# Performance work log

Hardware: AMD Instinct MI355X
Metric: run time of the kernel (lower is better)

## Reference

```python
import jax, jax.numpy as jnp
import numpy as np

THRESH = 8000.0  # saturating partial-sum accumulator threshold (thresh=8000 in source)
GROUP = 128      # channel chunk size used by split_tensor_* helpers
EPS = 1e-5

def binarize(x):
    # sign() forward with straight-through estimator (standard BinarizeConv2d behavior)
    return x + jax.lax.stop_gradient(jnp.sign(x) - x)

def psum_conv3x3(x, w):
    """3x3 'same' conv computed as 9 shifted-window partial sums per 128-channel
    group, with the running accumulator saturated to [-THRESH, THRESH] after each
    partial sum (emulating a low-bit hardware accumulator).
    x: [B, C, H, W]; w: [O, C, 3, 3] -> out [B, O, H, W]."""
    B, C, H, W = x.shape
    O = w.shape[0]
    xp = jnp.pad(x, ((0, 0), (0, 0), (1, 1), (1, 1)))
    acc = jnp.zeros((B, O, H, W), dtype=x.dtype)
    n_groups = C // GROUP
    for g in range(n_groups):
        xg = xp[:, g * GROUP:(g + 1) * GROUP]
        wg = w[:, g * GROUP:(g + 1) * GROUP]
        # split_tensor ordering: x1..x9 vary row (dim2) fastest, then col (dim3)
        for col in range(3):
            for row in range(3):
                part = jnp.einsum('bchw,oc->bohw',
                                  xg[:, :, row:row + H, col:col + W],
                                  wg[:, :, row, col])
                acc = jnp.clip(acc + part, -THRESH, THRESH)
    return acc

def batchnorm(x, gamma, beta, mean, var):
    inv = gamma / jnp.sqrt(var + EPS)
    return x * inv[None, :, None, None] + (beta - mean * inv)[None, :, None, None]

def setup_inputs() -> dict:
    key = jax.random.key(0)
    ks = jax.random.split(key, 12)
    B, C, H, W = 64, 128, 56, 56
    return {
        'x': jax.random.normal(ks[0], (B, C, H, W), jnp.float32),
        'w1': jax.random.normal(ks[1], (C, C, 3, 3), jnp.float32),
        'w2': jax.random.normal(ks[2], (C, C, 3, 3), jnp.float32),
        'gamma1': jax.random.uniform(ks[3], (C,), jnp.float32, 0.5, 1.5),
        'beta1': jax.random.normal(ks[4], (C,), jnp.float32) * 0.1,
        'mean1': jax.random.normal(ks[5], (C,), jnp.float32),
        'var1': jax.random.uniform(ks[6], (C,), jnp.float32, 0.5, 1.5),
        'gamma2': jax.random.uniform(ks[7], (C,), jnp.float32, 0.5, 1.5),
        'beta2': jax.random.normal(ks[8], (C,), jnp.float32) * 0.1,
        'mean2': jax.random.normal(ks[9], (C,), jnp.float32),
        'var2': jax.random.uniform(ks[10], (C,), jnp.float32, 0.5, 1.5),
    }

def reference(x, w1, w2, gamma1, beta1, mean1, var1, gamma2, beta2, mean2, var2):
    residual = x
    out = psum_conv3x3(binarize(x), binarize(w1))
    out = batchnorm(out, gamma1, beta1, mean1, var1)
    out = jnp.clip(out, -1.0, 1.0)  # hardtanh
    out = psum_conv3x3(binarize(out), binarize(w2))
    out = batchnorm(out, gamma2, beta2, mean2, var2)
    out = out + residual
    out = jnp.clip(out, -1.0, 1.0)
    return out
```

## Files before the change

kernel.cpp:

```cpp
#include <hip/hip_runtime.h>
#include <cstdint>
#include <cstddef>


typedef int      v4i __attribute__((ext_vector_type(4)));
typedef float    v4f __attribute__((ext_vector_type(4)));
typedef unsigned int v2u __attribute__((ext_vector_type(2)));

constexpr int B = 64, C = 128, H = 56, W = 56;
constexpr int HP = H + 2, WP = W + 2;
constexpr int PIX = H * W;
constexpr int M = B * H * W;
constexpr int NTILES = M / 256;
constexpr int TPX = NTILES / 8;

constexpr size_t XS_BYTES = (size_t)B * HP * WP * C;
constexpr size_t XS1_OFF = 0;
constexpr size_t XS2_OFF = XS_BYTES;
constexpr size_t WF_BYTES = 18 * 8192;
constexpr size_t WF1_OFF = 2 * XS_BYTES;
constexpr size_t WF2_OFF = WF1_OFF + WF_BYTES;
constexpr size_t BNP_OFF = WF2_OFF + WF_BYTES;

__global__ __launch_bounds__(256) void zero_halo(int8_t* __restrict__ xs1,
                                                 int8_t* __restrict__ xs2) {
    int b = blockIdx.x >> 2;
    int q = blockIdx.x & 3;
    int t = q * 256 + threadIdx.x;
    size_t ib = (size_t)b * HP * WP * C;
#pragma unroll
    for (int a = 0; a < 2; ++a) {
        uint32_t* p = (uint32_t*)((a ? xs2 : xs1) + ib);
        const int ROWD = WP * C / 4;
        for (int i = t; i < ROWD; i += 1024) {
            p[i] = 0;
            p[(HP - 1) * ROWD + i] = 0;
        }
        for (int i = t; i < 56 * 2 * 32; i += 1024) {
            int r = i >> 6;
            int side = (i >> 5) & 1;
            int j = i & 31;
            p[((r + 1) * WP + side * (WP - 1)) * (C / 4) + j] = 0;
        }
    }
}

__global__ __launch_bounds__(256) void prep_x(const float* __restrict__ x,
                                              int8_t* __restrict__ xs) {
    __shared__ uint32_t tl[256 * 33];
    int t = threadIdx.x;
    int m = blockIdx.x * 256 + t;
    int b_ = m / PIX, hw = m % PIX;
    const float* xp = x + (size_t)b_ * C * PIX + hw;
#pragma unroll
    for (int c4 = 0; c4 < 32; ++c4) {
        uint32_t v = 0;
#pragma unroll
        for (int j = 0; j < 4; ++j) {
            float f = __builtin_nontemporal_load(xp + (size_t)(c4 * 4 + j) * PIX);
            v |= ((uint32_t)(uint8_t)(int8_t)((f > 0.f) - (f < 0.f))) << (8 * j);
        }
        tl[t * 33 + c4] = v;
    }
    __syncthreads();
    int pl = t >> 3, co = t & 7;
#pragma unroll
    for (int pass = 0; pass < 8; ++pass) {
        int p = pass * 32 + pl;
        int mg = blockIdx.x * 256 + p;
        int b2 = mg / PIX, hw2 = mg % PIX, h2 = hw2 / W, w2 = hw2 % W;
        size_t ob = ((size_t)(b2 * HP + h2 + 1) * WP + (w2 + 1)) * C + co * 16;
        v4i val;
#pragma unroll
        for (int k = 0; k < 4; ++k) val[k] = (int)tl[p * 33 + co * 4 + k];
        *(v4i*)(xs + ob) = val;
    }
}

__global__ __launch_bounds__(256) void prep_w(
    const float* __restrict__ w1, const float* __restrict__ w2,
    const float* __restrict__ g1, const float* __restrict__ be1,
    const float* __restrict__ mu1, const float* __restrict__ va1,
    const float* __restrict__ g2, const float* __restrict__ be2,
    const float* __restrict__ mu2, const float* __restrict__ va2,
    int8_t* __restrict__ wf1, int8_t* __restrict__ wf2,
    float* __restrict__ bnp) {
    int t = blockIdx.x * 256 + threadIdx.x;
    if (t < 256) {
        int o = t & 127;
        if (t < 128) {
            float inv = g1[o] / sqrtf(va1[o] + 1e-5f);
            bnp[o]       = inv;
            bnp[128 + o] = __fsub_rn(be1[o], __fmul_rn(mu1[o], inv));
        } else {
            float inv = g2[o] / sqrtf(va2[o] + 1e-5f);
            bnp[256 + o] = inv;
            bnp[384 + o] = __fsub_rn(be2[o], __fmul_rn(mu2[o], inv));
        }
    }
    if (t >= 2 * 18 * 8 * 64) return;
    int lane = t & 63;
    int nsub = (t >> 6) & 7;
    int kh   = (t >> 9) & 1;
    int tap  = (t >> 10) % 9;
    int which = (t >> 10) / 9;
    const float* w = which ? w2 : w1;
    int8_t* wf = which ? wf2 : wf1;
    int o = (lane & 15) * 8 + nsub;
    int cbase = kh * 64 + (lane >> 4) * 16;
    int r = tap / 3, s = tap % 3;
    int slot = r * 6 + kh * 3 + s;
    int8_t frag[16];
#pragma unroll
    for (int j = 0; j < 16; ++j) {
        float f = w[((size_t)(o * C + cbase + j) * 3 + r) * 3 + s];
        frag[j] = (int8_t)((f > 0.f) - (f < 0.f));
    }
    *(v4i*)(wf + (size_t)((slot * 8 + nsub) * 64 + lane) * 16) =
        *(const v4i*)frag;
}

template <int RG>
__device__ __forceinline__ void do_conv(
    const int (&mrows)[RG], const int8_t* __restrict__ xs, const int8_t* wlds,
    int lane, int quad, int l15, v4i (&acc)[RG][8])
{
    int abase[RG];
#pragma unroll
    for (int rg = 0; rg < RG; ++rg) {
        int ma = mrows[rg] + l15;
        int wa = ma % W; int ta = ma / W; int ha = ta % H; int ba = ta / H;
        abase[rg] = ((ba * HP + ha) * WP + wa) * C + quad * 16;
    }
    int lidx = lane << 4;

#pragma unroll
    for (int rg = 0; rg < RG; ++rg)
#pragma unroll
        for (int n = 0; n < 8; ++n) acc[rg][n] = (v4i)0;

    v4i a0[RG], a1[RG], bf0[8], bf1[8];
#pragma unroll
    for (int rg = 0; rg < RG; ++rg) a0[rg] = *(const v4i*)(xs + abase[rg]);
#pragma unroll
    for (int n = 0; n < 8; ++n)
        bf0[n] = *(const v4i*)(wlds + n * 1024 + lidx);
    __builtin_amdgcn_sched_barrier(0);

    const int8_t* wl = wlds;
    int aoffr = 0;
#pragma unroll 1
    for (int r3 = 0; r3 < 3; ++r3) {
#pragma unroll
        for (int kk = 0; kk < 6; ++kk) {
            const bool last = (r3 == 2) && (kk == 5);
            if (!last) {
                const int nkh = (kk + 1 < 6) ? ((kk + 1) / 3) : 0;
                const int ns  = (kk + 1 < 6) ? ((kk + 1) % 3) : 0;
                const int rbump = (kk + 1 < 6) ? 0 : WP * C;
                int naoff = aoffr + rbump + nkh * 64 + ns * C;
                const int8_t* lb = wl + (kk + 1) * 8192;
                if (((kk + 1) & 1) == 0) {
#pragma unroll
                    for (int rg = 0; rg < RG; ++rg)
                        a0[rg] = *(const v4i*)(xs + abase[rg] + naoff);
#pragma unroll
                    for (int n = 0; n < 8; ++n)
                        bf0[n] = *(const v4i*)(lb + n * 1024 + lidx);
                } else {
#pragma unroll
                    for (int rg = 0; rg < RG; ++rg)
                        a1[rg] = *(const v4i*)(xs + abase[rg] + naoff);
#pragma unroll
                    for (int n = 0; n < 8; ++n)
                        bf1[n] = *(const v4i*)(lb + n * 1024 + lidx);
                }
            }
            __builtin_amdgcn_sched_barrier(0);
            __builtin_amdgcn_s_setprio(1);
            if ((kk & 1) == 0) {
#pragma unroll
                for (int n = 0; n < 8; ++n)
#pragma unroll
                    for (int rg = 0; rg < RG; ++rg)
                        acc[rg][n] = __builtin_amdgcn_mfma_i32_16x16x64_i8(
                            a0[rg], bf0[n], acc[rg][n], 0, 0, 0);
            } else {
#pragma unroll
                for (int n = 0; n < 8; ++n)
#pragma unroll
                    for (int rg = 0; rg < RG; ++rg)
                        acc[rg][n] = __builtin_amdgcn_mfma_i32_16x16x64_i8(
                            a1[rg], bf1[n], acc[rg][n], 0, 0, 0);
            }
            __builtin_amdgcn_s_setprio(0);
            __builtin_amdgcn_sched_barrier(0);
        }
        aoffr += WP * C;
        wl += 6 * 8192;
    }
}

template <int RG>
__device__ __forceinline__ void epi_p1(
    v4i (&acc)[RG][8], const int (&mrows)[RG], int quad, int l15,
    const float* binv, const float* btt, int8_t* __restrict__ xs_next)
{
#pragma unroll
    for (int rg = 0; rg < RG; ++rg) {
        int m0 = mrows[rg] + quad * 4;
        int w0 = m0 % W; int t0 = m0 / W; int h0 = t0 % H; int b0 = t0 / H;
        int base = ((b0 * HP + h0 + 1) * WP + (w0 + 1)) * C + l15 * 8;
#pragma unroll
        for (int i = 0; i < 4; ++i) {
            uint32_t lo = 0, hi = 0;
#pragma unroll
            for (int n = 0; n < 8; ++n) {
                float y = __fadd_rn(__fmul_rn((float)acc[rg][n][i], binv[n]), btt[n]);
                uint32_t sb = (uint8_t)(int8_t)((y > 0.f) - (y < 0.f));
                if (n < 4) lo |= sb << (8 * n);
                else       hi |= sb << (8 * (n - 4));
            }
            v2u pk; pk[0] = lo; pk[1] = hi;
            *(v2u*)(xs_next + base + i * C) = pk;
        }
    }
}

template <int RG>
__device__ __forceinline__ void epi_p2(
    v4i (&acc)[RG][8], const int (&mrows)[RG], int quad, int l15,
    const float* binv, const float* btt,
    const float* __restrict__ xres, float* __restrict__ out)
{
#pragma unroll
    for (int rg = 0; rg < RG; ++rg) {
        int m0 = mrows[rg] + quad * 4;
        int w0 = m0 % W; int t0 = m0 / W; int h0 = t0 % H; int b0 = t0 / H;
        int pixb = b0 * C * PIX + h0 * W + w0;
#pragma unroll
        for (int n = 0; n < 8; ++n) {
            int idx = pixb + (l15 * 8 + n) * PIX;
            v4f r = __builtin_nontemporal_load((const v4f*)(xres + idx));
            v4f z;
#pragma unroll
            for (int i = 0; i < 4; ++i) {
                float y = __fadd_rn(__fmul_rn((float)acc[rg][n][i], binv[n]), btt[n]);
                float v = __fadd_rn(y, r[i]);
                z[i] = fminf(fmaxf(v, -1.f), 1.f);
            }
            __builtin_nontemporal_store(z, (v4f*)(out + idx));
        }
    }
}

__global__ __attribute__((amdgpu_flat_work_group_size(512, 512)))
__attribute__((amdgpu_waves_per_eu(2, 2))) void conv_p1(
    const int8_t* __restrict__ xs,
    const int8_t* __restrict__ wf,
    const float* __restrict__ bnp,
    int8_t* __restrict__ xs_next)
{
    __shared__ int8_t wlds[18 * 8192];
    int t = threadIdx.x, lane = t & 63, wv = t >> 6;
    int quad = lane >> 4, l15 = lane & 15;

    {
        const v4i* g = (const v4i*)wf;
        v4i* l = (v4i*)wlds;
        for (int i = t; i < 18 * 512; i += 512) l[i] = g[i];
    }
    float binv[8], btt[8];
    {
        int o0 = l15 * 8, o1 = 128 + l15 * 8;
#pragma unroll
        for (int n = 0; n < 8; ++n) { binv[n] = bnp[o0 + n]; btt[n] = bnp[o1 + n]; }
    }
    __syncthreads();

    int xcd = blockIdx.x & 7, local = blockIdx.x >> 3;
#pragma unroll 1
    for (int rd = 0; rd < 2; ++rd) {
        int mw = (xcd * TPX + local + rd * 32) * 256 + wv * 32;
        int mrows2[2] = { mw, mw + 16 };
        v4i acc[2][8];
        do_conv<2>(mrows2, xs, wlds, lane, quad, l15, acc);
        epi_p1<2>(acc, mrows2, quad, l15, binv, btt, xs_next);
    }
    {
        int mw = (xcd * TPX + local + 64) * 256 + wv * 32;
        if (local < 4) {
            int tailrow = (xcd * TPX + 96) * 256 + (local * 8 + wv) * 16;
            int mrows3[3] = { mw, mw + 16, tailrow };
            v4i acc[3][8];
            do_conv<3>(mrows3, xs, wlds, lane, quad, l15, acc);
            epi_p1<3>(acc, mrows3, quad, l15, binv, btt, xs_next);
        } else {
            int mrows2[2] = { mw, mw + 16 };
            v4i acc[2][8];
            do_conv<2>(mrows2, xs, wlds, lane, quad, l15, acc);
            epi_p1<2>(acc, mrows2, quad, l15, binv, btt, xs_next);
        }
    }
}

__global__ __attribute__((amdgpu_flat_work_group_size(512, 512)))
__attribute__((amdgpu_waves_per_eu(2, 2))) void conv_p2(
    const int8_t* __restrict__ xs,
    const int8_t* __restrict__ wf,
    const float* __restrict__ bnp,
    const float* __restrict__ xres,
    float* __restrict__ out)
{
    __shared__ int8_t wlds[18 * 8192];
    int t = threadIdx.x, lane = t & 63, wv = t >> 6;
    int quad = lane >> 4, l15 = lane & 15;

    {
        const v4i* g = (const v4i*)wf;
        v4i* l = (v4i*)wlds;
        for (int i = t; i < 18 * 512; i += 512) l[i] = g[i];
    }
    float binv[8], btt[8];
    {
        int o0 = 256 + l15 * 8, o1 = 384 + l15 * 8;
#pragma unroll
        for (int n = 0; n < 8; ++n) { binv[n] = bnp[o0 + n]; btt[n] = bnp[o1 + n]; }
    }
    __syncthreads();

    int xcd = blockIdx.x & 7, local = blockIdx.x >> 3;
#pragma unroll 1
    for (int rd = 0; rd < 2; ++rd) {
        int mw = (xcd * TPX + local + rd * 32) * 256 + wv * 32;
        int mrows2[2] = { mw, mw + 16 };
        v4i acc[2][8];
        do_conv<2>(mrows2, xs, wlds, lane, quad, l15, acc);
        epi_p2<2>(acc, mrows2, quad, l15, binv, btt, xres, out);
    }
    {
        int mw = (xcd * TPX + local + 64) * 256 + wv * 32;
        if (local < 4) {
            int tailrow = (xcd * TPX + 96) * 256 + (local * 8 + wv) * 16;
            int mrows3[3] = { mw, mw + 16, tailrow };
            v4i acc[3][8];
            do_conv<3>(mrows3, xs, wlds, lane, quad, l15, acc);
            epi_p2<3>(acc, mrows3, quad, l15, binv, btt, xres, out);
        } else {
            int mrows2[2] = { mw, mw + 16 };
            v4i acc[2][8];
            do_conv<2>(mrows2, xs, wlds, lane, quad, l15, acc);
            epi_p2<2>(acc, mrows2, quad, l15, binv, btt, xres, out);
        }
    }
}

extern "C" void kernel_launch(void* const* d_in, const int* in_sizes, int n_in,
                              void* d_out, int out_size, void* d_ws, size_t ws_size,
                              hipStream_t stream) {
    const float* x   = (const float*)d_in[0];
    const float* w1  = (const float*)d_in[1];
    const float* w2  = (const float*)d_in[2];
    const float* g1  = (const float*)d_in[3];
    const float* be1 = (const float*)d_in[4];
    const float* mu1 = (const float*)d_in[5];
    const float* va1 = (const float*)d_in[6];
    const float* g2  = (const float*)d_in[7];
    const float* be2 = (const float*)d_in[8];
    const float* mu2 = (const float*)d_in[9];
    const float* va2 = (const float*)d_in[10];

    int8_t* ws  = (int8_t*)d_ws;
    int8_t* xs1 = ws + XS1_OFF;
    int8_t* xs2 = ws + XS2_OFF;
    int8_t* wf1 = ws + WF1_OFF;
    int8_t* wf2 = ws + WF2_OFF;
    float*  bnp = (float*)(ws + BNP_OFF);

    zero_halo<<<256, 256, 0, stream>>>(xs1, xs2);
    prep_x<<<M / 256, 256, 0, stream>>>(x, xs1);
    prep_w<<<(2 * 18 * 8 * 64 + 255) / 256, 256, 0, stream>>>(
        w1, w2, g1, be1, mu1, va1, g2, be2, mu2, va2, wf1, wf2, bnp);

    conv_p1<<<256, 512, 0, stream>>>(xs1, wf1, bnp, xs2);
    conv_p2<<<256, 512, 0, stream>>>(xs2, wf2, bnp, x, (float*)d_out);
}
```

Measured before the change: 332.1 us.

## Triple-buffer activation loads with inline asm and explicit vmcnt waits

Replaces the double-buffered activation fragment loads with a three-deep rotation issued via inline-asm global loads, using explicit s_waitcnt vmcnt so that two taps of global latency stay in flight while MFMAs run. The tail-tile handling also changes from a 3-row-group pass on a few blocks to a separate single-row-group pass, so the main loop always uses two row groups. Launch bounds switch to __launch_bounds__(512,1), which drops the waves_per_eu(2,2) hint and may change register allocation and occupancy. Hand-written vmcnt counts depend on the compiler not emitting other vector memory ops in between, so correctness relies on the scheduling barriers holding.

Measured after the change: 323.8 us. 1.03x faster.

```diff
diff --git a/kernel.cpp b/kernel.cpp
--- a/kernel.cpp
+++ b/kernel.cpp
@@ -120,17 +120,25 @@
         *(const v4i*)frag;
 }
 
+template <int N>
+__device__ __forceinline__ void wait_vm() {
+    if constexpr (N == 0) asm volatile("s_waitcnt vmcnt(0)");
+    else if constexpr (N == 2) asm volatile("s_waitcnt vmcnt(2)");
+    else if constexpr (N == 4) asm volatile("s_waitcnt vmcnt(4)");
+    else if constexpr (N == 6) asm volatile("s_waitcnt vmcnt(6)");
+}
+
 template <int RG>
 __device__ __forceinline__ void do_conv(
     const int (&mrows)[RG], const int8_t* __restrict__ xs, const int8_t* wlds,
     int lane, int quad, int l15, v4i (&acc)[RG][8])
 {
-    int abase[RG];
+    const int8_t* ap[RG];
 #pragma unroll
     for (int rg = 0; rg < RG; ++rg) {
         int ma = mrows[rg] + l15;
         int wa = ma % W; int ta = ma / W; int ha = ta % H; int ba = ta / H;
-        abase[rg] = ((ba * HP + ha) * WP + wa) * C + quad * 16;
+        ap[rg] = xs + ((ba * HP + ha) * WP + wa) * C + quad * 16;
     }
     int lidx = lane << 4;
 
@@ -139,9 +147,17 @@
 #pragma unroll
         for (int n = 0; n < 8; ++n) acc[rg][n] = (v4i)0;
 
-    v4i a0[RG], a1[RG], bf0[8], bf1[8];
-#pragma unroll
-    for (int rg = 0; rg < RG; ++rg) a0[rg] = *(const v4i*)(xs + abase[rg]);
+    v4i a[3][RG];
+    v4i bf0[8], bf1[8];
+
+#pragma unroll
+    for (int rg = 0; rg < RG; ++rg)
+        asm volatile("global_load_dwordx4 %0, %1, off"
+                     : "=v"(a[0][rg]) : "v"(ap[rg]));
+#pragma unroll
+    for (int rg = 0; rg < RG; ++rg)
+        asm volatile("global_load_dwordx4 %0, %1, off"
+                     : "=v"(a[1][rg]) : "v"(ap[rg] + C));
 #pragma unroll
     for (int n = 0; n < 8; ++n)
         bf0[n] = *(const v4i*)(wlds + n * 1024 + lidx);
@@ -153,30 +169,33 @@
     for (int r3 = 0; r3 < 3; ++r3) {
 #pragma unroll
         for (int kk = 0; kk < 6; ++kk) {
-            const bool last = (r3 == 2) && (kk == 5);
-            if (!last) {
-                const int nkh = (kk + 1 < 6) ? ((kk + 1) / 3) : 0;
-                const int ns  = (kk + 1 < 6) ? ((kk + 1) % 3) : 0;
-                const int rbump = (kk + 1 < 6) ? 0 : WP * C;
-                int naoff = aoffr + rbump + nkh * 64 + ns * C;
+            if (kk <= 3 || r3 != 2) {
+                const int kp = (kk + 2) % 6;
+                const int rb = (kk <= 3) ? 0 : WP * C;
+                const int noff = rb + (kp / 3) * 64 + (kp % 3) * C;
+#pragma unroll
+                for (int rg = 0; rg < RG; ++rg) {
+                    const int8_t* p = ap[rg] + aoffr + noff;
+                    asm volatile("global_load_dwordx4 %0, %1, off"
+                                 : "=v"(a[(kk + 2) % 3][rg]) : "v"(p));
+                }
+            }
+            if (kk < 5 || r3 != 2) {
                 const int8_t* lb = wl + (kk + 1) * 8192;
                 if (((kk + 1) & 1) == 0) {
-#pragma unroll
-                    for (int rg = 0; rg < RG; ++rg)
-                        a0[rg] = *(const v4i*)(xs + abase[rg] + naoff);
 #pragma unroll
                     for (int n = 0; n < 8; ++n)
                         bf0[n] = *(const v4i*)(lb + n * 1024 + lidx);
                 } else {
 #pragma unroll
-                    for (int rg = 0; rg < RG; ++rg)
-                        a1[rg] = *(const v4i*)(xs + abase[rg] + naoff);
-#pragma unroll
                     for (int n = 0; n < 8; ++n)
                         bf1[n] = *(const v4i*)(lb + n * 1024 + lidx);
                 }
             }
             __builtin_amdgcn_sched_barrier(0);
+            if (r3 == 2 && kk >= 4) wait_vm<0>();
+            else                    wait_vm<2 * RG>();
+            __builtin_amdgcn_sched_barrier(0);
             __builtin_amdgcn_s_setprio(1);
             if ((kk & 1) == 0) {
 #pragma unroll
@@ -184,14 +203,14 @@
 #pragma unroll
                     for (int rg = 0; rg < RG; ++rg)
                         acc[rg][n] = __builtin_amdgcn_mfma_i32_16x16x64_i8(
-                            a0[rg], bf0[n], acc[rg][n], 0, 0, 0);
+                            a[kk % 3][rg], bf0[n], acc[rg][n], 0, 0, 0);
             } else {
 #pragma unroll
                 for (int n = 0; n < 8; ++n)
 #pragma unroll
                     for (int rg = 0; rg < RG; ++rg)
                         acc[rg][n] = __builtin_amdgcn_mfma_i32_16x16x64_i8(
-                            a1[rg], bf1[n], acc[rg][n], 0, 0, 0);
+                            a[kk % 3][rg], bf1[n], acc[rg][n], 0, 0, 0);
             }
             __builtin_amdgcn_s_setprio(0);
             __builtin_amdgcn_sched_barrier(0);
@@ -254,8 +273,7 @@
     }
 }
 
-__global__ __attribute__((amdgpu_flat_work_group_size(512, 512)))
-__attribute__((amdgpu_waves_per_eu(2, 2))) void conv_p1(
+__global__ __launch_bounds__(512, 1) void conv_p1(
     const int8_t* __restrict__ xs,
     const int8_t* __restrict__ wf,
     const float* __restrict__ bnp,
@@ -280,32 +298,24 @@
 
     int xcd = blockIdx.x & 7, local = blockIdx.x >> 3;
 #pragma unroll 1
-    for (int rd = 0; rd < 2; ++rd) {
-        int mw = (xcd * TPX + local + rd * 32) * 256 + wv * 32;
+    for (int tloc = local; tloc < 96; tloc += 32) {
+        int mw = (xcd * TPX + tloc) * 256 + wv * 32;
         int mrows2[2] = { mw, mw + 16 };
         v4i acc[2][8];
         do_conv<2>(mrows2, xs, wlds, lane, quad, l15, acc);
         epi_p1<2>(acc, mrows2, quad, l15, binv, btt, xs_next);
     }
-    {
-        int mw = (xcd * TPX + local + 64) * 256 + wv * 32;
-        if (local < 4) {
-            int tailrow = (xcd * TPX + 96) * 256 + (local * 8 + wv) * 16;
-            int mrows3[3] = { mw, mw + 16, tailrow };
-            v4i acc[3][8];
-            do_conv<3>(mrows3, xs, wlds, lane, quad, l15, acc);
-            epi_p1<3>(acc, mrows3, quad, l15, binv, btt, xs_next);
-        } else {
-            int mrows2[2] = { mw, mw + 16 };
-            v4i acc[2][8];
-            do_conv<2>(mrows2, xs, wlds, lane, quad, l15, acc);
-            epi_p1<2>(acc, mrows2, quad, l15, binv, btt, xs_next);
-        }
-    }
-}
-
-__global__ __attribute__((amdgpu_flat_work_group_size(512, 512)))
-__attribute__((amdgpu_waves_per_eu(2, 2))) void conv_p2(
+    if (local < 4) {
+        int tile = xcd * TPX + 96 + (local >> 1);
+        int mw = tile * 256 + (local & 1) * 128 + wv * 16;
+        int mrows1[1] = { mw };
+        v4i acc[1][8];
+        do_conv<1>(mrows1, xs, wlds, lane, quad, l15, acc);
+        epi_p1<1>(acc, mrows1, quad, l15, binv, btt, xs_next);
+    }
+}
+
+__global__ __launch_bounds__(512, 1) void conv_p2(
     const int8_t* __restrict__ xs,
     const int8_t* __restrict__ wf,
     const float* __restrict__ bnp,
@@ -331,27 +341,20 @@
 
     int xcd = blockIdx.x & 7, local = blockIdx.x >> 3;
 #pragma unroll 1
-    for (int rd = 0; rd < 2; ++rd) {
-        int mw = (xcd * TPX + local + rd * 32) * 256 + wv * 32;
+    for (int tloc = local; tloc < 96; tloc += 32) {
+        int mw = (xcd * TPX + tloc) * 256 + wv * 32;
         int mrows2[2] = { mw, mw + 16 };
         v4i acc[2][8];
         do_conv<2>(mrows2, xs, wlds, lane, quad, l15, acc);
         epi_p2<2>(acc, mrows2, quad, l15, binv, btt, xres, out);
     }
-    {
-        int mw = (xcd * TPX + local + 64) * 256 + wv * 32;
-        if (local < 4) {
-            int tailrow = (xcd * TPX + 96) * 256 + (local * 8 + wv) * 16;
-            int mrows3[3] = { mw, mw + 16, tailrow };
-            v4i acc[3][8];
-            do_conv<3>(mrows3, xs, wlds, lane, quad, l15, acc);
-            epi_p2<3>(acc, mrows3, quad, l15, binv, btt, xres, out);
-        } else {
-            int mrows2[2] = { mw, mw + 16 };
-            v4i acc[2][8];
-            do_conv<2>(mrows2, xs, wlds, lane, quad, l15, acc);
-            epi_p2<2>(acc, mrows2, quad, l15, binv, btt, xres, out);
-        }
+    if (local < 4) {
+        int tile = xcd * TPX + 96 + (local >> 1);
+        int mw = tile * 256 + (local & 1) * 128 + wv * 16;
+        int mrows1[1] = { mw };
+        v4i acc[1][8];
+        do_conv<1>(mrows1, xs, wlds, lane, quad, l15, acc);
+        epi_p2<1>(acc, mrows1, quad, l15, binv, btt, xres, out);
     }
 }
 
```
